# Optimization experiments

Measured on AMD Instinct MI355X. Metric: run time of the kernel, lower is better.

The kernel has to match this reference:

```python
import jax, jax.numpy as jnp
import numpy as np

B, S, HID = 2, 2048, 4096
NH, NKV, D = 32, 8, 128
GROUPS = NH // NKV  # 4 query heads per KV head
THETA = 10000.0
MAX_SEQ = 4096


def _rope_tables():
    half = D // 2
    inv_freq = 1.0 / (THETA ** (np.arange(half, dtype=np.float32) / half))
    t = np.arange(MAX_SEQ, dtype=np.float32)
    freqs = np.outer(t, inv_freq)  # [MAX_SEQ, D//2]
    return jnp.asarray(np.cos(freqs)), jnp.asarray(np.sin(freqs))

ROPE_COS, ROPE_SIN = _rope_tables()


def _apply_rope(x, cos, sin):
    # x: [B, S, H, D]; cos/sin: [S, D//2]; half-split (NeoX) rotation as in _apply_rope_inline
    half = x.shape[-1] // 2
    x0, x1 = x[..., :half], x[..., half:]
    c = cos[None, :, None, :]
    s = sin[None, :, None, :]
    return jnp.concatenate([x0 * c - x1 * s, x0 * s + x1 * c], axis=-1)


def setup_inputs() -> dict:
    key = jax.random.key(0)
    ks = jax.random.split(key, 5)
    wscale = 1.0 / np.sqrt(HID).astype(np.float32)  # keep activations O(1)
    return {
        "x": jax.random.normal(ks[0], (B, S, HID), dtype=jnp.float32),
        "positions": jnp.arange(S, dtype=jnp.int32),
        "w_q": jax.random.normal(ks[1], (NH * D, HID), dtype=jnp.float32) * wscale,
        "w_k": jax.random.normal(ks[2], (NKV * D, HID), dtype=jnp.float32) * wscale,
        "w_v": jax.random.normal(ks[3], (NKV * D, HID), dtype=jnp.float32) * wscale,
        "w_o": jax.random.normal(ks[4], (HID, NH * D), dtype=jnp.float32) * wscale,
    }


def reference(x, positions, w_q, w_k, w_v, w_o):
    cos = ROPE_COS[positions]  # [S, D//2]
    sin = ROPE_SIN[positions]
    # Separate Q/K/V projections (no bias), as in the training forward()
    q = (x @ w_q.T).reshape(B, S, NH, D)
    k = (x @ w_k.T).reshape(B, S, NKV, D)
    v = (x @ w_v.T).reshape(B, S, NKV, D)
    q = _apply_rope(q, cos, sin)
    k = _apply_rope(k, cos, sin)
    # [B, H, S, D] layout
    q = q.transpose(0, 2, 1, 3)
    k = k.transpose(0, 2, 1, 3)
    v = v.transpose(0, 2, 1, 3)
    # GQA: group query heads over shared KV heads instead of repeating K/V
    qg = q.reshape(B, NKV, GROUPS, S, D)
    scale = 1.0 / jnp.sqrt(jnp.float32(D))
    scores = jnp.einsum("bkgqd,bkmd->bkgqm", qg, k) * scale  # [B, NKV, G, Sq, Skv]
    causal = jnp.tril(jnp.ones((S, S), dtype=bool))
    scores = jnp.where(causal[None, None, None], scores, jnp.float32(-jnp.inf))
    probs = jax.nn.softmax(scores, axis=-1)
    ctx = jnp.einsum("bkgqm,bkmd->bkgqd", probs, v)  # [B, NKV, G, S, D]
    ctx = ctx.reshape(B, NH, S, D).transpose(0, 2, 1, 3).reshape(B, S, NH * D)
    return ctx @ w_o.T
```

## Files before the change

kernel.cpp:

```cpp
#include <hip/hip_runtime.h>
#include <math.h>

typedef short s16x8 __attribute__((ext_vector_type(8)));
typedef float f32x4 __attribute__((ext_vector_type(4)));
typedef unsigned u32x4 __attribute__((ext_vector_type(4)));
typedef unsigned short u16;

#define S_LEN 2048
#define HID_DIM 4096
#define NH_Q 32
#define NKV_H 8
#define DHEAD 128

__device__ __forceinline__ u16 f2bf(float f) {
  unsigned u = __builtin_bit_cast(unsigned, f);
  u += 0x7fffu + ((u >> 16) & 1u);
  return (u16)(u >> 16);
}

__device__ __forceinline__ void gload16(const u16* g, u16* l) {
  __builtin_amdgcn_global_load_lds(
      (const __attribute__((address_space(1))) void*)g,
      (__attribute__((address_space(3))) void*)l, 16, 0, 0);
}

__global__ void cvt_kernel(const float* __restrict__ in, u16* __restrict__ out, int n4) {
  int stride = gridDim.x * blockDim.x;
  for (int i = blockIdx.x * blockDim.x + threadIdx.x; i < n4; i += stride) {
    float4 f = ((const float4*)in)[i];
    uint2 o;
    o.x = (unsigned)f2bf(f.x) | ((unsigned)f2bf(f.y) << 16);
    o.y = (unsigned)f2bf(f.z) | ((unsigned)f2bf(f.w) << 16);
    ((uint2*)out)[i] = o;
  }
}

__global__ void rope_table_kernel(const int* __restrict__ positions,
                                  float* __restrict__ cos_t, float* __restrict__ sin_t) {
  int idx = blockIdx.x * 256 + threadIdx.x;
  if (idx >= S_LEN * 64) return;
  int s = idx >> 6, j = idx & 63;
  float pos = (float)positions[s];
  float inv = expf(-(float)j * (9.210340371976184f / 64.0f));
  float ang = pos * inv;
  float sv, cv;
  sincosf(ang, &sv, &cv);
  cos_t[idx] = cv;
  sin_t[idx] = sv;
}

template<int EPI>
__global__ __launch_bounds__(512) void gemm8p_kernel(
    const u16* __restrict__ A, const u16* __restrict__ B,
    void* __restrict__ outp, int M, int N, int K,
    const float* __restrict__ cos_t, const float* __restrict__ sin_t) {
  __shared__ u16 AsL[2][8192];
  __shared__ u16 BsL[2][8192];
  const int t = threadIdx.x;
  const int wave = t >> 6, lane = t & 63;
  const int l15 = lane & 15, lhi = lane >> 4;
  const int wr = wave >> 2, wc = wave & 3;
  const int gx = gridDim.x;
  const int nwg = gx * gridDim.y;
  const int id = blockIdx.y * gx + blockIdx.x;
  const int swz = (id & 7) * (nwg >> 3) + (id >> 3);
  const int bm = (swz / gx) * 256, bn = (swz % gx) * 256;

  const int srow = t >> 2;
  const int scol = 8 * ((t & 3) ^ ((t >> 3) & 3));
  const size_t ga0 = (size_t)(bm + srow) * K + scol;
  const size_t ga1 = (size_t)(bm + 128 + srow) * K + scol;
  const size_t gb0 = (size_t)(bn + srow) * K + scol;
  const size_t gb1 = (size_t)(bn + 128 + srow) * K + scol;
  const int ldst = wave * 512;

  const int slotA = (lhi ^ ((l15 >> 1) & 3)) << 3;
  const int aidx = wr * 4096 + l15 * 32 + slotA;
  int bidx[4];
#pragma unroll
  for (int nf = 0; nf < 4; ++nf)
    bidx[nf] = (nf >> 1) * 4096 + (wc * 16 + (nf & 1) * 64 + l15) * 32 + slotA;

  const f32x4 fz = {0.f, 0.f, 0.f, 0.f};
  f32x4 acc[8][4];
#pragma unroll
  for (int mf = 0; mf < 8; ++mf)
#pragma unroll
    for (int nf = 0; nf < 4; ++nf) acc[mf][nf] = fz;

  auto stage = [&](int tt) {
    const int b = tt & 1;
    const int kt = tt << 5;
    gload16(A + ga0 + kt, &AsL[b][ldst]);
    gload16(A + ga1 + kt, &AsL[b][4096 + ldst]);
    gload16(B + gb0 + kt, &BsL[b][ldst]);
    gload16(B + gb1 + kt, &BsL[b][4096 + ldst]);
  };

  const int nt = K >> 5;
  stage(0);
  asm volatile("s_waitcnt vmcnt(0)" ::: "memory");
  __builtin_amdgcn_s_barrier();

  for (int tt = 0; tt < nt; ++tt) {
    const u16* Ab = &AsL[tt & 1][0];
    const u16* Bb = &BsL[tt & 1][0];
    s16x8 af[4], bf[4];
#pragma unroll
    for (int mf = 0; mf < 4; ++mf) af[mf] = *(const s16x8*)&Ab[aidx + mf * 512];
#pragma unroll
    for (int nf = 0; nf < 4; ++nf) bf[nf] = *(const s16x8*)&Bb[bidx[nf]];
    if (tt + 1 < nt) stage(tt + 1);
    __builtin_amdgcn_s_barrier();
    __builtin_amdgcn_s_setprio(1);
#pragma unroll
    for (int mf = 0; mf < 4; ++mf)
#pragma unroll
      for (int nf = 0; nf < 4; ++nf)
        acc[mf][nf] = __builtin_amdgcn_mfma_f32_16x16x32_bf16(af[mf], bf[nf], acc[mf][nf], 0, 0, 0);
    __builtin_amdgcn_s_setprio(0);
    __builtin_amdgcn_s_barrier();
#pragma unroll
    for (int mf = 0; mf < 4; ++mf) af[mf] = *(const s16x8*)&Ab[aidx + (mf + 4) * 512];
    __builtin_amdgcn_s_barrier();
    __builtin_amdgcn_s_setprio(1);
#pragma unroll
    for (int mf = 0; mf < 4; ++mf)
#pragma unroll
      for (int nf = 0; nf < 4; ++nf)
        acc[mf + 4][nf] =
            __builtin_amdgcn_mfma_f32_16x16x32_bf16(af[mf], bf[nf], acc[mf + 4][nf], 0, 0, 0);
    __builtin_amdgcn_s_setprio(0);
    asm volatile("s_waitcnt vmcnt(0)" ::: "memory");
    __builtin_amdgcn_s_barrier();
  }

  if (EPI == 0) {
    float* C = (float*)outp;
#pragma unroll
    for (int mf = 0; mf < 8; ++mf) {
      int rb = bm + wr * 128 + mf * 16 + lhi * 4;
#pragma unroll
      for (int nf = 0; nf < 4; ++nf) {
        int col = bn + wc * 16 + nf * 64 + l15;
#pragma unroll
        for (int i = 0; i < 4; ++i) C[(size_t)(rb + i) * N + col] = acc[mf][nf][i];
      }
    }
  } else {
    u16* qp = (u16*)outp;
    u16* kp = qp + 16777216;
    u16* vp = kp + 4194304;
    if (bn < 4096 || (bn >= 4096 && bn < 5120)) {
      const bool isQ = bn < 4096;
      u16* O = isQ ? qp : kp;
      const int hb = isQ ? (bn >> 7) : ((bn - 4096) >> 7);
      const int Hh = isQ ? NH_Q : NKV_H;
      const int j = wc * 16 + l15;
#pragma unroll
      for (int mf = 0; mf < 8; ++mf) {
        int rb = bm + wr * 128 + mf * 16 + lhi * 4;
#pragma unroll
        for (int p = 0; p < 2; ++p) {
          int head = hb + p;
#pragma unroll
          for (int i = 0; i < 4; ++i) {
            int m = rb + i;
            int b = m >> 11, srw = m & 2047;
            float c = cos_t[srw * 64 + j];
            float s = sin_t[srw * 64 + j];
            float x0 = acc[mf][2 * p][i];
            float x1 = acc[mf][2 * p + 1][i];
            size_t base = ((size_t)(b * Hh + head) * S_LEN + srw) * DHEAD;
            O[base + j] = f2bf(x0 * c - x1 * s);
            O[base + j + 64] = f2bf(x0 * s + x1 * c);
          }
        }
      }
    } else {
#pragma unroll
      for (int mf = 0; mf < 8; ++mf) {
        int rb = bm + wr * 128 + mf * 16 + lhi * 4;
#pragma unroll
        for (int nf = 0; nf < 4; ++nf) {
          int colrel = bn - 5120 + wc * 16 + nf * 64 + l15;
          int head = colrel >> 7, d = colrel & 127;
#pragma unroll
          for (int i = 0; i < 4; ++i) {
            int m = rb + i;
            int b = m >> 11, srw = m & 2047;
            vp[((size_t)(b * NKV_H + head) * DHEAD + d) * S_LEN + srw] = f2bf(acc[mf][nf][i]);
          }
        }
      }
    }
  }
}

template<int EPI, bool ABF16, bool BBF16>
__global__ __launch_bounds__(256) void gemm_kernel(
    const void* __restrict__ Aptr, const void* __restrict__ Bptr,
    void* __restrict__ outp, void* __restrict__ outp2, int M, int N, int K,
    const float* __restrict__ cos_t, const float* __restrict__ sin_t, int Hh) {
  __shared__ u16 As[128][72];
  __shared__ u16 Bs[128][72];
  const int t = threadIdx.x;
  const int wave = t >> 6, lane = t & 63;
  const int l15 = lane & 15, lhi = lane >> 4;
  const int gx = gridDim.x;
  const int nwg = gx * gridDim.y;
  const int id = blockIdx.y * gx + blockIdx.x;
  const int swz = (id & 7) * (nwg >> 3) + (id >> 3);
  const int bm = (swz / gx) * 128, bn = (swz % gx) * 128;

  const f32x4 fz = {0.f, 0.f, 0.f, 0.f};
  f32x4 acc[2][8];
#pragma unroll
  for (int a0 = 0; a0 < 2; ++a0)
#pragma unroll
    for (int b0 = 0; b0 < 8; ++b0) acc[a0][b0] = fz;

  for (int kt = 0; kt < K; kt += 64) {
    __syncthreads();
    if (ABF16) {
      const u16* A = (const u16*)Aptr;
#pragma unroll
      for (int p = 0; p < 4; ++p) {
        int row = p * 32 + (t >> 3), kc = (t & 7) * 8;
        *(s16x8*)&As[row][kc] = *(const s16x8*)(A + (size_t)(bm + row) * K + kt + kc);
      }
    } else {
      const float* A = (const float*)Aptr;
#pragma unroll
      for (int p = 0; p < 8; ++p) {
        int row = p * 16 + (t >> 4), kc = (t & 15) * 4;
        float4 f = *(const float4*)(A + (size_t)(bm + row) * K + kt + kc);
        unsigned* dst = (unsigned*)&As[row][kc];
        dst[0] = (unsigned)f2bf(f.x) | ((unsigned)f2bf(f.y) << 16);
        dst[1] = (unsigned)f2bf(f.z) | ((unsigned)f2bf(f.w) << 16);
      }
    }
    if (BBF16) {
      const u16* Bw = (const u16*)Bptr;
#pragma unroll
      for (int p = 0; p < 4; ++p) {
        int row = p * 32 + (t >> 3), kc = (t & 7) * 8;
        *(s16x8*)&Bs[row][kc] = *(const s16x8*)(Bw + (size_t)(bn + row) * K + kt + kc);
      }
    } else {
      const float* Bw = (const float*)Bptr;
#pragma unroll
      for (int p = 0; p < 8; ++p) {
        int row = p * 16 + (t >> 4), kc = (t & 15) * 4;
        float4 f = *(const float4*)(Bw + (size_t)(bn + row) * K + kt + kc);
        unsigned* dst = (unsigned*)&Bs[row][kc];
        dst[0] = (unsigned)f2bf(f.x) | ((unsigned)f2bf(f.y) << 16);
        dst[1] = (unsigned)f2bf(f.z) | ((unsigned)f2bf(f.w) << 16);
      }
    }
    __syncthreads();
#pragma unroll
    for (int ks = 0; ks < 2; ++ks) {
      s16x8 bfr[8];
#pragma unroll
      for (int nf = 0; nf < 8; ++nf)
        bfr[nf] = *(const s16x8*)&Bs[nf * 16 + l15][ks * 32 + lhi * 8];
#pragma unroll
      for (int mf = 0; mf < 2; ++mf) {
        s16x8 a = *(const s16x8*)&As[wave * 32 + mf * 16 + l15][ks * 32 + lhi * 8];
#pragma unroll
        for (int nf = 0; nf < 8; ++nf)
          acc[mf][nf] = __builtin_amdgcn_mfma_f32_16x16x32_bf16(a, bfr[nf], acc[mf][nf], 0, 0, 0);
      }
    }
  }

  if (EPI == 0) {
    float* C = (float*)outp;
#pragma unroll
    for (int mf = 0; mf < 2; ++mf)
#pragma unroll
      for (int nf = 0; nf < 8; ++nf) {
        int col = bn + nf * 16 + l15;
        int rb = bm + wave * 32 + mf * 16 + lhi * 4;
#pragma unroll
        for (int i = 0; i < 4; ++i) C[(size_t)(rb + i) * N + col] = acc[mf][nf][i];
      }
  } else if (EPI == 2) {
    u16* O = (u16*)outp;
    int h = bn >> 7;
#pragma unroll
    for (int mf = 0; mf < 2; ++mf)
#pragma unroll
      for (int nf = 0; nf < 4; ++nf) {
        int j = nf * 16 + l15;
        int rb = bm + wave * 32 + mf * 16 + lhi * 4;
#pragma unroll
        for (int i = 0; i < 4; ++i) {
          int m = rb + i;
          int b = m >> 11, srow = m & 2047;
          float c = cos_t[srow * 64 + j];
          float s = sin_t[srow * 64 + j];
          float x0 = acc[mf][nf][i];
          float x1 = acc[mf][nf + 4][i];
          size_t base = ((size_t)(b * Hh + h) * S_LEN + srow) * DHEAD;
          O[base + j] = f2bf(x0 * c - x1 * s);
          O[base + j + 64] = f2bf(x0 * s + x1 * c);
        }
      }
  } else {
    u16* O = (u16*)outp;
#pragma unroll
    for (int mf = 0; mf < 2; ++mf)
#pragma unroll
      for (int nf = 0; nf < 8; ++nf) {
        int col = bn + nf * 16 + l15;
        int h = col >> 7, d = col & 127;
        int rb = bm + wave * 32 + mf * 16 + lhi * 4;
#pragma unroll
        for (int i = 0; i < 4; ++i) {
          int m = rb + i;
          int b = m >> 11, srow = m & 2047;
          O[((size_t)(b * Hh + h) * DHEAD + d) * S_LEN + srow] = f2bf(acc[mf][nf][i]);
        }
      }
  }
}

#define KIDX(r, c) (((r) * 128 + (c)) ^ (((r) & 7) << 3))
#define VIDX(d, kv) (((d) * 64 + (kv)) ^ (((d) & 7) << 3))
__global__ __launch_bounds__(512) void attn_kernel(
    const u16* __restrict__ q, const u16* __restrict__ k, const u16* __restrict__ vt,
    u16* __restrict__ ctx) {
  __shared__ u16 Ks[64 * 128];
  __shared__ u16 Vts[128 * 64];

  const int t = threadIdx.x;
  const int wave = t >> 6, lane = t & 63;
  const int l15 = lane & 15, lhi = lane >> 4;
  const int pi = blockIdx.x, h = blockIdx.y, b = blockIdx.z;
  const int kvh = h >> 2;
  const int qsub[2] = {pi, 15 - pi};
  const int ntiles = 32 - 2 * pi;

  const u16* qb = q + ((size_t)(b * NH_Q + h)) * S_LEN * DHEAD;
  const u16* kb = k + ((size_t)(b * NKV_H + kvh)) * S_LEN * DHEAD;
  const u16* vtb = vt + ((size_t)(b * NKV_H + kvh)) * DHEAD * S_LEN;

  s16x8 qf[2][4];
#pragma unroll
  for (int s = 0; s < 2; ++s)
#pragma unroll
    for (int ks = 0; ks < 4; ++ks)
      qf[s][ks] = *(const s16x8*)(qb + (size_t)(qsub[s] * 128 + wave * 16 + l15) * DHEAD +
                                  ks * 32 + lhi * 8);

  const f32x4 fz = {0.f, 0.f, 0.f, 0.f};
  f32x4 acc[2][8];
#pragma unroll
  for (int s = 0; s < 2; ++s)
#pragma unroll
    for (int i = 0; i < 8; ++i) acc[s][i] = fz;
  float mrow[2] = {-INFINITY, -INFINITY};
  float lsum[2] = {0.f, 0.f};

  const float scale = 0.08838834764831845f;

  const int sl0 = l15 | (((2 * lhi) & 3) << 4);
  const int sl1 = sl0 | 16;
  const bool hisel = (lhi & 2) != 0;

  const int krow = t >> 3, kd0 = (t & 7) * 16;
  const int vrow = t >> 2, vk0 = (t & 3) * 16;
  s16x8 kr0, kr1, vr0, vr1;
  {
    const u16* p = kb + (size_t)krow * DHEAD + kd0;
    kr0 = *(const s16x8*)p;
    kr1 = *(const s16x8*)(p + 8);
    const u16* pv = vtb + (size_t)vrow * S_LEN + vk0;
    vr0 = *(const s16x8*)pv;
    vr1 = *(const s16x8*)(pv + 8);
  }

  for (int tt = 0; tt < ntiles; ++tt) {
    __syncthreads();
    *(s16x8*)&Ks[KIDX(krow, kd0)] = kr0;
    *(s16x8*)&Ks[KIDX(krow, kd0 + 8)] = kr1;
    *(s16x8*)&Vts[VIDX(vrow, vk0)] = vr0;
    *(s16x8*)&Vts[VIDX(vrow, vk0 + 8)] = vr1;
    __syncthreads();
    if (tt + 1 < ntiles) {
      const u16* p = kb + (size_t)((tt + 1) * 64 + krow) * DHEAD + kd0;
      kr0 = *(const s16x8*)p;
      kr1 = *(const s16x8*)(p + 8);
      const u16* pv = vtb + (size_t)vrow * S_LEN + (tt + 1) * 64 + vk0;
      vr0 = *(const s16x8*)pv;
      vr1 = *(const s16x8*)(pv + 8);
    }

    const int kc_base = tt * 64;
#pragma unroll
    for (int s = 0; s < 2; ++s) {
      const int wmin = qsub[s] * 128 + wave * 16;
      if (kc_base > wmin + 15) continue;
      f32x4 sacc[4];
#pragma unroll
      for (int i = 0; i < 4; ++i) sacc[i] = fz;
      __builtin_amdgcn_s_setprio(1);
#pragma unroll
      for (int ks = 0; ks < 4; ++ks) {
#pragma unroll
        for (int nf = 0; nf < 4; ++nf) {
          s16x8 kf = *(const s16x8*)&Ks[KIDX(nf * 16 + l15, ks * 32 + lhi * 8)];
          sacc[nf] = __builtin_amdgcn_mfma_f32_16x16x32_bf16(kf, qf[s][ks], sacc[nf], 0, 0, 0);
        }
      }
      __builtin_amdgcn_s_setprio(0);

      const int qg = wmin + l15;
      float pmax = -INFINITY;
      if (kc_base + 63 > wmin) {
#pragma unroll
        for (int nf = 0; nf < 4; ++nf)
#pragma unroll
          for (int i = 0; i < 4; ++i) {
            int kv = kc_base + nf * 16 + lhi * 4 + i;
            float sv = sacc[nf][i] * scale;
            sv = (kv <= qg) ? sv : -INFINITY;
            sacc[nf][i] = sv;
            pmax = fmaxf(pmax, sv);
          }
      } else {
#pragma unroll
        for (int nf = 0; nf < 4; ++nf)
#pragma unroll
          for (int i = 0; i < 4; ++i) {
            float sv = sacc[nf][i] * scale;
            sacc[nf][i] = sv;
            pmax = fmaxf(pmax, sv);
          }
      }
      pmax = fmaxf(pmax, __shfl_xor(pmax, 16, 64));
      pmax = fmaxf(pmax, __shfl_xor(pmax, 32, 64));

      if (!__all(pmax <= mrow[s] + 8.0f)) {
        float mnew = fmaxf(mrow[s], pmax);
        float alpha = __expf(mrow[s] - mnew);
        mrow[s] = mnew;
        lsum[s] *= alpha;
#pragma unroll
        for (int i = 0; i < 4; ++i) {
          float al = __shfl(alpha, (lane & 48) | (lhi * 4 + i), 64);
#pragma unroll
          for (int df = 0; df < 8; ++df) acc[s][df][i] *= al;
        }
      }

      float rsum = 0.f;
      unsigned pk[4][2];
#pragma unroll
      for (int nf = 0; nf < 4; ++nf) {
        float p0 = __expf(sacc[nf][0] - mrow[s]);
        float p1 = __expf(sacc[nf][1] - mrow[s]);
        float p2 = __expf(sacc[nf][2] - mrow[s]);
        float p3 = __expf(sacc[nf][3] - mrow[s]);
        rsum += (p0 + p1) + (p2 + p3);
        pk[nf][0] = (unsigned)f2bf(p0) | ((unsigned)f2bf(p1) << 16);
        pk[nf][1] = (unsigned)f2bf(p2) | ((unsigned)f2bf(p3) << 16);
      }
      rsum += __shfl_xor(rsum, 16, 64);
      rsum += __shfl_xor(rsum, 32, 64);
      lsum[s] += rsum;

      s16x8 pa[2];
#pragma unroll
      for (int ph = 0; ph < 2; ++ph) {
        unsigned lo0 = __shfl((int)pk[2 * ph][0], sl0, 64);
        unsigned hi0 = __shfl((int)pk[2 * ph + 1][0], sl0, 64);
        unsigned lo1 = __shfl((int)pk[2 * ph][1], sl0, 64);
        unsigned hi1 = __shfl((int)pk[2 * ph + 1][1], sl0, 64);
        unsigned lo2 = __shfl((int)pk[2 * ph][0], sl1, 64);
        unsigned hi2 = __shfl((int)pk[2 * ph + 1][0], sl1, 64);
        unsigned lo3 = __shfl((int)pk[2 * ph][1], sl1, 64);
        unsigned hi3 = __shfl((int)pk[2 * ph + 1][1], sl1, 64);
        u32x4 w;
        w[0] = hisel ? hi0 : lo0;
        w[1] = hisel ? hi1 : lo1;
        w[2] = hisel ? hi2 : lo2;
        w[3] = hisel ? hi3 : lo3;
        pa[ph] = __builtin_bit_cast(s16x8, w);
      }

      __builtin_amdgcn_s_setprio(1);
#pragma unroll
      for (int ph = 0; ph < 2; ++ph) {
#pragma unroll
        for (int df = 0; df < 8; ++df) {
          s16x8 bb = *(const s16x8*)&Vts[VIDX(df * 16 + l15, ph * 32 + lhi * 8)];
          acc[s][df] = __builtin_amdgcn_mfma_f32_16x16x32_bf16(pa[ph], bb, acc[s][df], 0, 0, 0);
        }
      }
      __builtin_amdgcn_s_setprio(0);
    }
  }

#pragma unroll
  for (int s = 0; s < 2; ++s) {
    float rl = 1.0f / lsum[s];
#pragma unroll
    for (int i = 0; i < 4; ++i) {
      float rli = __shfl(rl, (lane & 48) | (lhi * 4 + i), 64);
      int m = b * S_LEN + qsub[s] * 128 + wave * 16 + lhi * 4 + i;
#pragma unroll
      for (int df = 0; df < 8; ++df) {
        int col = h * DHEAD + df * 16 + l15;
        ctx[(size_t)m * (NH_Q * DHEAD) + col] = f2bf(acc[s][df][i] * rli);
      }
    }
  }
}

extern "C" void kernel_launch(void* const* d_in, const int* in_sizes, int n_in,
                              void* d_out, int out_size, void* d_ws, size_t ws_size,
                              hipStream_t stream) {
  const float* x = (const float*)d_in[0];
  const int* positions = (const int*)d_in[1];
  const float* wq = (const float*)d_in[2];
  const float* wk = (const float*)d_in[3];
  const float* wv = (const float*)d_in[4];
  const float* wo = (const float*)d_in[5];
  float* out = (float*)d_out;

  char* ws = (char*)d_ws;
  const size_t MB1 = 1048576;
  const size_t SZ_X = 33554432;
  const size_t SZ_WQKV = 50331648;
  const size_t SZ_Q = 33554432;
  const size_t SZ_WK = 8388608;
  const size_t NEED_FULL = MB1 + SZ_X + SZ_WQKV + SZ_Q + 2 * SZ_WK;

  float* cos_t = (float*)ws;
  float* sin_t = (float*)(ws + MB1 / 2);

  rope_table_kernel<<<512, 256, 0, stream>>>(positions, cos_t, sin_t);

  if (ws_size >= NEED_FULL) {
    char* p = ws + MB1;
    u16* x_bf = (u16*)p;    p += SZ_X;
    u16* wqkv_bf = (u16*)p; p += SZ_WQKV;
    u16* q_ws = (u16*)p;    p += SZ_Q;
    u16* k_ws = (u16*)p;    p += SZ_WK;
    u16* v_ws = (u16*)p;    p += SZ_WK;
    u16* ctx_ws = x_bf;

    cvt_kernel<<<2048, 256, 0, stream>>>(x, x_bf, 4194304);
    cvt_kernel<<<2048, 256, 0, stream>>>(wq, wqkv_bf, 4194304);
    cvt_kernel<<<1024, 256, 0, stream>>>(wk, wqkv_bf + 16777216, 1048576);
    cvt_kernel<<<1024, 256, 0, stream>>>(wv, wqkv_bf + 20971520, 1048576);

    gemm8p_kernel<5><<<dim3(24, 16), 512, 0, stream>>>(
        x_bf, wqkv_bf, q_ws, 4096, 6144, 4096, cos_t, sin_t);
    cvt_kernel<<<2048, 256, 0, stream>>>(wo, wqkv_bf, 4194304);
    attn_kernel<<<dim3(8, 32, 2), 512, 0, stream>>>(q_ws, k_ws, v_ws, ctx_ws);
    gemm8p_kernel<0><<<dim3(16, 16), 512, 0, stream>>>(
        ctx_ws, wqkv_bf, out, 4096, 4096, 4096, nullptr, nullptr);
  } else {
    u16* q_ws = (u16*)(ws + MB1);
    u16* k_ws = (u16*)(ws + MB1 + SZ_Q);
    u16* v_ws = (u16*)(ws + MB1 + SZ_Q + SZ_WK);
    u16* ctx_ws = (u16*)(ws + MB1 + SZ_Q + 2 * SZ_WK);

    gemm_kernel<2, false, false><<<dim3(32, 32), 256, 0, stream>>>(
        x, wq, q_ws, nullptr, 4096, 4096, 4096, cos_t, sin_t, NH_Q);
    gemm_kernel<2, false, false><<<dim3(8, 32), 256, 0, stream>>>(
        x, wk, k_ws, nullptr, 4096, 1024, 4096, cos_t, sin_t, NKV_H);
    gemm_kernel<4, false, false><<<dim3(8, 32), 256, 0, stream>>>(
        x, wv, v_ws, nullptr, 4096, 1024, 4096, nullptr, nullptr, NKV_H);
    attn_kernel<<<dim3(8, 32, 2), 512, 0, stream>>>(q_ws, k_ws, v_ws, ctx_ws);
    gemm_kernel<0, true, false><<<dim3(32, 32), 256, 0, stream>>>(
        ctx_ws, wo, out, nullptr, 4096, 4096, 4096, nullptr, nullptr, 0);
  }
}
```

Measured before the change: 608.7 us.

## Triple-buffer GEMM LDS tiles with two-stage-ahead prefetch and fewer barriers

Replaces the double-buffered GEMM main loop with a three-buffer ring that prefetches two K-tiles ahead. Partial vmcnt waits replace the full drain, and the per-iteration barriers drop from four to two. The launch bound now requests two workgroups per CU. The aim is to hide global-load latency behind MFMA work and cut synchronisation stalls, at the cost of 96KB of LDS per block and extra register pressure from the occupancy hint.

```diff
diff --git a/kernel.cpp b/kernel.cpp
--- a/kernel.cpp
+++ b/kernel.cpp
@@ -50,12 +50,12 @@
 }
 
 template<int EPI>
-__global__ __launch_bounds__(512) void gemm8p_kernel(
+__global__ __launch_bounds__(512, 2) void gemmp2_kernel(
     const u16* __restrict__ A, const u16* __restrict__ B,
     void* __restrict__ outp, int M, int N, int K,
     const float* __restrict__ cos_t, const float* __restrict__ sin_t) {
-  __shared__ u16 AsL[2][8192];
-  __shared__ u16 BsL[2][8192];
+  __shared__ u16 AsL[3][8192];
+  __shared__ u16 BsL[3][8192];
   const int t = threadIdx.x;
   const int wave = t >> 6, lane = t & 63;
   const int l15 = lane & 15, lhi = lane >> 4;
@@ -88,30 +88,39 @@
 #pragma unroll
     for (int nf = 0; nf < 4; ++nf) acc[mf][nf] = fz;
 
-  auto stage = [&](int tt) {
-    const int b = tt & 1;
+  auto stage = [&](int tt, int buf) {
     const int kt = tt << 5;
-    gload16(A + ga0 + kt, &AsL[b][ldst]);
-    gload16(A + ga1 + kt, &AsL[b][4096 + ldst]);
-    gload16(B + gb0 + kt, &BsL[b][ldst]);
-    gload16(B + gb1 + kt, &BsL[b][4096 + ldst]);
+    gload16(A + ga0 + kt, &AsL[buf][ldst]);
+    gload16(A + ga1 + kt, &AsL[buf][4096 + ldst]);
+    gload16(B + gb0 + kt, &BsL[buf][ldst]);
+    gload16(B + gb1 + kt, &BsL[buf][4096 + ldst]);
   };
 
   const int nt = K >> 5;
-  stage(0);
-  asm volatile("s_waitcnt vmcnt(0)" ::: "memory");
-  __builtin_amdgcn_s_barrier();
-
+  stage(0, 0);
+  stage(1, 1);
+
+  int cur = 0, nxt2 = 2;
   for (int tt = 0; tt < nt; ++tt) {
-    const u16* Ab = &AsL[tt & 1][0];
-    const u16* Bb = &BsL[tt & 1][0];
-    s16x8 af[4], bf[4];
+    if (tt + 2 < nt) {
+      stage(tt + 2, nxt2);
+      asm volatile("s_waitcnt vmcnt(8)" ::: "memory");
+    } else if (tt + 1 < nt) {
+      asm volatile("s_waitcnt vmcnt(4)" ::: "memory");
+    } else {
+      asm volatile("s_waitcnt vmcnt(0)" ::: "memory");
+    }
+    __builtin_amdgcn_sched_barrier(0);
+    __builtin_amdgcn_s_barrier();
+    __builtin_amdgcn_sched_barrier(0);
+
+    const u16* Ab = &AsL[cur][0];
+    const u16* Bb = &BsL[cur][0];
+    s16x8 bf[4], af[4];
+#pragma unroll
+    for (int nf = 0; nf < 4; ++nf) bf[nf] = *(const s16x8*)&Bb[bidx[nf]];
 #pragma unroll
     for (int mf = 0; mf < 4; ++mf) af[mf] = *(const s16x8*)&Ab[aidx + mf * 512];
-#pragma unroll
-    for (int nf = 0; nf < 4; ++nf) bf[nf] = *(const s16x8*)&Bb[bidx[nf]];
-    if (tt + 1 < nt) stage(tt + 1);
-    __builtin_amdgcn_s_barrier();
     __builtin_amdgcn_s_setprio(1);
 #pragma unroll
     for (int mf = 0; mf < 4; ++mf)
@@ -119,10 +128,8 @@
       for (int nf = 0; nf < 4; ++nf)
         acc[mf][nf] = __builtin_amdgcn_mfma_f32_16x16x32_bf16(af[mf], bf[nf], acc[mf][nf], 0, 0, 0);
     __builtin_amdgcn_s_setprio(0);
-    __builtin_amdgcn_s_barrier();
 #pragma unroll
     for (int mf = 0; mf < 4; ++mf) af[mf] = *(const s16x8*)&Ab[aidx + (mf + 4) * 512];
-    __builtin_amdgcn_s_barrier();
     __builtin_amdgcn_s_setprio(1);
 #pragma unroll
     for (int mf = 0; mf < 4; ++mf)
@@ -131,8 +138,12 @@
         acc[mf + 4][nf] =
             __builtin_amdgcn_mfma_f32_16x16x32_bf16(af[mf], bf[nf], acc[mf + 4][nf], 0, 0, 0);
     __builtin_amdgcn_s_setprio(0);
-    asm volatile("s_waitcnt vmcnt(0)" ::: "memory");
+
+    asm volatile("s_waitcnt lgkmcnt(0)" ::: "memory");
+    __builtin_amdgcn_sched_barrier(0);
     __builtin_amdgcn_s_barrier();
+    cur = (cur == 2) ? 0 : cur + 1;
+    nxt2 = (nxt2 == 2) ? 0 : nxt2 + 1;
   }
 
   if (EPI == 0) {
@@ -151,7 +162,7 @@
     u16* qp = (u16*)outp;
     u16* kp = qp + 16777216;
     u16* vp = kp + 4194304;
-    if (bn < 4096 || (bn >= 4096 && bn < 5120)) {
+    if (bn < 5120) {
       const bool isQ = bn < 4096;
       u16* O = isQ ? qp : kp;
       const int hb = isQ ? (bn >> 7) : ((bn - 4096) >> 7);
@@ -558,11 +569,11 @@
     cvt_kernel<<<1024, 256, 0, stream>>>(wk, wqkv_bf + 16777216, 1048576);
     cvt_kernel<<<1024, 256, 0, stream>>>(wv, wqkv_bf + 20971520, 1048576);
 
-    gemm8p_kernel<5><<<dim3(24, 16), 512, 0, stream>>>(
+    gemmp2_kernel<5><<<dim3(24, 16), 512, 0, stream>>>(
         x_bf, wqkv_bf, q_ws, 4096, 6144, 4096, cos_t, sin_t);
     cvt_kernel<<<2048, 256, 0, stream>>>(wo, wqkv_bf, 4194304);
     attn_kernel<<<dim3(8, 32, 2), 512, 0, stream>>>(q_ws, k_ws, v_ws, ctx_ws);
-    gemm8p_kernel<0><<<dim3(16, 16), 512, 0, stream>>>(
+    gemmp2_kernel<0><<<dim3(16, 16), 512, 0, stream>>>(
         ctx_ws, wqkv_bf, out, 4096, 4096, 4096, nullptr, nullptr);
   } else {
     u16* q_ws = (u16*)(ws + MB1);
```

Result: slower. 668.3 us (+9.8%).

## Restructure bf16 GEMM into 8-phase pipeline with half-tile staging and K=64 tiles

Applied to the files above, without the earlier changes.

Rewrites the main bf16 GEMM mainloop to use a single 128KB LDS buffer holding K=64 double-buffered tiles split into halves. Each of eight phases reads a quarter of the A/B fragments while a half-tile load for the next iteration is in flight, with barriers and fine-grained vmcnt waits in between. The LDS XOR swizzle moves to an 8-way pattern, and launch bounds now request 2 blocks per CU. The aim is to keep MFMA issue continuous by overlapping global loads and LDS reads with compute. In exchange there are more barriers per iteration and higher LDS use, which may limit occupancy.

```diff
diff --git a/kernel.cpp b/kernel.cpp
--- a/kernel.cpp
+++ b/kernel.cpp
@@ -50,12 +50,11 @@
 }
 
 template<int EPI>
-__global__ __launch_bounds__(512) void gemm8p_kernel(
+__global__ __launch_bounds__(512, 2) void gemm8ph_kernel(
     const u16* __restrict__ A, const u16* __restrict__ B,
     void* __restrict__ outp, int M, int N, int K,
     const float* __restrict__ cos_t, const float* __restrict__ sin_t) {
-  __shared__ u16 AsL[2][8192];
-  __shared__ u16 BsL[2][8192];
+  __shared__ u16 LDS[65536];
   const int t = threadIdx.x;
   const int wave = t >> 6, lane = t & 63;
   const int l15 = lane & 15, lhi = lane >> 4;
@@ -66,20 +65,24 @@
   const int swz = (id & 7) * (nwg >> 3) + (id >> 3);
   const int bm = (swz / gx) * 256, bn = (swz % gx) * 256;
 
-  const int srow = t >> 2;
-  const int scol = 8 * ((t & 3) ^ ((t >> 3) & 3));
-  const size_t ga0 = (size_t)(bm + srow) * K + scol;
-  const size_t ga1 = (size_t)(bm + 128 + srow) * K + scol;
-  const size_t gb0 = (size_t)(bn + srow) * K + scol;
-  const size_t gb1 = (size_t)(bn + 128 + srow) * K + scol;
-  const int ldst = wave * 512;
-
-  const int slotA = (lhi ^ ((l15 >> 1) & 3)) << 3;
-  const int aidx = wr * 4096 + l15 * 32 + slotA;
-  int bidx[4];
-#pragma unroll
-  for (int nf = 0; nf < 4; ++nf)
-    bidx[nf] = (nf >> 1) * 4096 + (wc * 16 + (nf & 1) * 64 + l15) * 32 + slotA;
+  const int sw = l15 & 7;
+  int aoff[4][2], boff[2][2];
+#pragma unroll
+  for (int q = 0; q < 4; ++q)
+#pragma unroll
+    for (int ks = 0; ks < 2; ++ks)
+      aoff[q][ks] = (wr * 64 + q * 16 + l15) * 64 + (((ks << 2) + lhi) ^ sw) * 8;
+#pragma unroll
+  for (int f = 0; f < 2; ++f)
+#pragma unroll
+    for (int ks = 0; ks < 2; ++ks)
+      boff[f][ks] = (f * 64 + wc * 16 + l15) * 64 + (((ks << 2) + lhi) ^ sw) * 8;
+
+  const int lr1 = t >> 3;
+  const int cs1 = ((t & 7) ^ (lr1 & 7)) * 8;
+  const int rA1 = lr1;
+  const int rA2 = 128 + lr1;
+  const int ldsw = wave * 512;
 
   const f32x4 fz = {0.f, 0.f, 0.f, 0.f};
   f32x4 acc[8][4];
@@ -88,70 +91,108 @@
 #pragma unroll
     for (int nf = 0; nf < 4; ++nf) acc[mf][nf] = fz;
 
-  auto stage = [&](int tt) {
-    const int b = tt & 1;
-    const int kt = tt << 5;
-    gload16(A + ga0 + kt, &AsL[b][ldst]);
-    gload16(A + ga1 + kt, &AsL[b][4096 + ldst]);
-    gload16(B + gb0 + kt, &BsL[b][ldst]);
-    gload16(B + gb1 + kt, &BsL[b][4096 + ldst]);
+  auto stageA = [&](int tile, int h, int buf) {
+    const size_t kb = (size_t)tile * 64;
+    gload16(A + (size_t)(bm + h * 64 + rA1) * K + kb + cs1,
+            &LDS[buf * 16384 + h * 8192 + ldsw]);
+    gload16(A + (size_t)(bm + h * 64 + rA2) * K + kb + cs1,
+            &LDS[buf * 16384 + h * 8192 + 4096 + ldsw]);
   };
-
-  const int nt = K >> 5;
-  stage(0);
-  asm volatile("s_waitcnt vmcnt(0)" ::: "memory");
+  auto stageB = [&](int tile, int h, int buf) {
+    const size_t kb = (size_t)tile * 64;
+    gload16(B + (size_t)(bn + h * 128 + lr1) * K + kb + cs1,
+            &LDS[32768 + buf * 16384 + h * 8192 + ldsw]);
+    gload16(B + (size_t)(bn + h * 128 + 64 + lr1) * K + kb + cs1,
+            &LDS[32768 + buf * 16384 + h * 8192 + 4096 + ldsw]);
+  };
+
+  s16x8 afr[4][2], bfr[2][2];
+  auto readA = [&](int mfH, int buf) {
+    const int base = buf * 16384 + mfH * 8192;
+#pragma unroll
+    for (int q = 0; q < 4; ++q)
+#pragma unroll
+      for (int ks = 0; ks < 2; ++ks)
+        afr[q][ks] = *(const s16x8*)&LDS[base + aoff[q][ks]];
+  };
+  auto readB = [&](int nfH, int buf) {
+    const int base = 32768 + buf * 16384 + nfH * 8192;
+#pragma unroll
+    for (int f = 0; f < 2; ++f)
+#pragma unroll
+      for (int ks = 0; ks < 2; ++ks)
+        bfr[f][ks] = *(const s16x8*)&LDS[base + boff[f][ks]];
+  };
+  auto mfma16 = [&](int mfH, int nfH) {
+    __builtin_amdgcn_s_setprio(1);
+#pragma unroll
+    for (int q = 0; q < 4; ++q)
+#pragma unroll
+      for (int f = 0; f < 2; ++f)
+#pragma unroll
+        for (int ks = 0; ks < 2; ++ks)
+          acc[mfH * 4 + q][nfH * 2 + f] = __builtin_amdgcn_mfma_f32_16x16x32_bf16(
+              afr[q][ks], bfr[f][ks], acc[mfH * 4 + q][nfH * 2 + f], 0, 0, 0);
+    __builtin_amdgcn_s_setprio(0);
+  };
+
+#define PHASE_SYNC()                        \
+  do {                                      \
+    __builtin_amdgcn_s_barrier();           \
+    asm volatile("s_waitcnt lgkmcnt(0)");   \
+    __builtin_amdgcn_sched_barrier(0);      \
+  } while (0)
+
+  stageA(0, 0, 0); stageB(0, 0, 0); stageA(0, 1, 0); stageB(0, 1, 0);
+  stageA(1, 0, 1); stageB(1, 1, 1);
+  asm volatile("s_waitcnt vmcnt(4)");
+  __builtin_amdgcn_sched_barrier(0);
   __builtin_amdgcn_s_barrier();
 
-  for (int tt = 0; tt < nt; ++tt) {
-    const u16* Ab = &AsL[tt & 1][0];
-    const u16* Bb = &BsL[tt & 1][0];
-    s16x8 af[4], bf[4];
-#pragma unroll
-    for (int mf = 0; mf < 4; ++mf) af[mf] = *(const s16x8*)&Ab[aidx + mf * 512];
-#pragma unroll
-    for (int nf = 0; nf < 4; ++nf) bf[nf] = *(const s16x8*)&Bb[bidx[nf]];
-    if (tt + 1 < nt) stage(tt + 1);
-    __builtin_amdgcn_s_barrier();
-    __builtin_amdgcn_s_setprio(1);
-#pragma unroll
-    for (int mf = 0; mf < 4; ++mf)
-#pragma unroll
-      for (int nf = 0; nf < 4; ++nf)
-        acc[mf][nf] = __builtin_amdgcn_mfma_f32_16x16x32_bf16(af[mf], bf[nf], acc[mf][nf], 0, 0, 0);
-    __builtin_amdgcn_s_setprio(0);
-    __builtin_amdgcn_s_barrier();
-#pragma unroll
-    for (int mf = 0; mf < 4; ++mf) af[mf] = *(const s16x8*)&Ab[aidx + (mf + 4) * 512];
-    __builtin_amdgcn_s_barrier();
-    __builtin_amdgcn_s_setprio(1);
-#pragma unroll
-    for (int mf = 0; mf < 4; ++mf)
-#pragma unroll
-      for (int nf = 0; nf < 4; ++nf)
-        acc[mf + 4][nf] =
-            __builtin_amdgcn_mfma_f32_16x16x32_bf16(af[mf], bf[nf], acc[mf + 4][nf], 0, 0, 0);
-    __builtin_amdgcn_s_setprio(0);
-    asm volatile("s_waitcnt vmcnt(0)" ::: "memory");
-    __builtin_amdgcn_s_barrier();
-  }
-
-  if (EPI == 0) {
+  const int nt = K >> 6;
+  for (int i = 0; i < (nt >> 1); ++i) {
+    const int t1 = 2 * i + 1, t2 = 2 * i + 2, t3 = 2 * i + 3;
+    const bool s2 = t2 < nt, s3 = t3 < nt;
+    readA(0, 0); readB(0, 0); stageA(t1, 1, 1);
+    PHASE_SYNC(); mfma16(0, 0); __builtin_amdgcn_s_barrier();
+    readB(1, 0); stageB(t1, 0, 1);
+    PHASE_SYNC(); mfma16(0, 1); __builtin_amdgcn_s_barrier();
+    readA(1, 0); if (s2) stageA(t2, 0, 0);
+    PHASE_SYNC(); mfma16(1, 1); __builtin_amdgcn_s_barrier();
+    readB(0, 0); if (s2) stageB(t2, 1, 0);
+    if (s2) { asm volatile("s_waitcnt vmcnt(4)"); }
+    else    { asm volatile("s_waitcnt vmcnt(0)"); }
+    PHASE_SYNC(); mfma16(1, 0); __builtin_amdgcn_s_barrier();
+    readA(0, 1); readB(0, 1); if (s2) stageA(t2, 1, 0);
+    PHASE_SYNC(); mfma16(0, 0); __builtin_amdgcn_s_barrier();
+    readB(1, 1); if (s2) stageB(t2, 0, 0);
+    PHASE_SYNC(); mfma16(0, 1); __builtin_amdgcn_s_barrier();
+    readA(1, 1); if (s3) stageA(t3, 0, 1);
+    PHASE_SYNC(); mfma16(1, 1); __builtin_amdgcn_s_barrier();
+    readB(0, 1); if (s3) stageB(t3, 1, 1);
+    if (s3) { asm volatile("s_waitcnt vmcnt(4)"); }
+    else    { asm volatile("s_waitcnt vmcnt(0)"); }
+    PHASE_SYNC(); mfma16(1, 0); __builtin_amdgcn_s_barrier();
+  }
+#undef PHASE_SYNC
+
+  if constexpr (EPI == 0) {
     float* C = (float*)outp;
 #pragma unroll
     for (int mf = 0; mf < 8; ++mf) {
       int rb = bm + wr * 128 + mf * 16 + lhi * 4;
 #pragma unroll
-      for (int nf = 0; nf < 4; ++nf) {
-        int col = bn + wc * 16 + nf * 64 + l15;
-#pragma unroll
-        for (int i = 0; i < 4; ++i) C[(size_t)(rb + i) * N + col] = acc[mf][nf][i];
+      for (int nfi = 0; nfi < 4; ++nfi) {
+        int col = bn + wc * 16 + (nfi & 1) * 64 + (nfi >> 1) * 128 + l15;
+#pragma unroll
+        for (int i = 0; i < 4; ++i) C[(size_t)(rb + i) * N + col] = acc[mf][nfi][i];
       }
     }
   } else {
     u16* qp = (u16*)outp;
     u16* kp = qp + 16777216;
     u16* vp = kp + 4194304;
-    if (bn < 4096 || (bn >= 4096 && bn < 5120)) {
+    if (bn < 5120) {
       const bool isQ = bn < 4096;
       u16* O = isQ ? qp : kp;
       const int hb = isQ ? (bn >> 7) : ((bn - 4096) >> 7);
@@ -182,14 +223,14 @@
       for (int mf = 0; mf < 8; ++mf) {
         int rb = bm + wr * 128 + mf * 16 + lhi * 4;
 #pragma unroll
-        for (int nf = 0; nf < 4; ++nf) {
-          int colrel = bn - 5120 + wc * 16 + nf * 64 + l15;
+        for (int nfi = 0; nfi < 4; ++nfi) {
+          int colrel = bn - 5120 + wc * 16 + (nfi & 1) * 64 + (nfi >> 1) * 128 + l15;
           int head = colrel >> 7, d = colrel & 127;
 #pragma unroll
           for (int i = 0; i < 4; ++i) {
             int m = rb + i;
             int b = m >> 11, srw = m & 2047;
-            vp[((size_t)(b * NKV_H + head) * DHEAD + d) * S_LEN + srw] = f2bf(acc[mf][nf][i]);
+            vp[((size_t)(b * NKV_H + head) * DHEAD + d) * S_LEN + srw] = f2bf(acc[mf][nfi][i]);
           }
         }
       }
@@ -558,11 +599,11 @@
     cvt_kernel<<<1024, 256, 0, stream>>>(wk, wqkv_bf + 16777216, 1048576);
     cvt_kernel<<<1024, 256, 0, stream>>>(wv, wqkv_bf + 20971520, 1048576);
 
-    gemm8p_kernel<5><<<dim3(24, 16), 512, 0, stream>>>(
+    gemm8ph_kernel<5><<<dim3(24, 16), 512, 0, stream>>>(
         x_bf, wqkv_bf, q_ws, 4096, 6144, 4096, cos_t, sin_t);
     cvt_kernel<<<2048, 256, 0, stream>>>(wo, wqkv_bf, 4194304);
     attn_kernel<<<dim3(8, 32, 2), 512, 0, stream>>>(q_ws, k_ws, v_ws, ctx_ws);
-    gemm8p_kernel<0><<<dim3(16, 16), 512, 0, stream>>>(
+    gemm8ph_kernel<0><<<dim3(16, 16), 512, 0, stream>>>(
         ctx_ws, wqkv_bf, out, 4096, 4096, 4096, nullptr, nullptr);
   } else {
     u16* q_ws = (u16*)(ws + MB1);
```

Result: faster. 540.6 us (-11.2%).
